# Kernel tuning notes

Hardware: AMD Instinct MI355X
Metric: run time of the kernel (lower is better)

## Reference

```python
import jax, jax.numpy as jnp
import numpy as np

NEG_SLOPE = 0.2
MASK_FILL = -1e9

N, F_IN, K, F_OUT = 4096, 512, 8, 128


def setup_inputs() -> dict:
    key = jax.random.key(0)
    k1, k2, k3, k4, k5 = jax.random.split(key, 5)
    x = jax.random.normal(k1, (N, F_IN), dtype=jnp.float32)
    mask = jax.random.randint(k2, (N, N), 0, 2).astype(jnp.bool_)
    # ensure no fully-masked row (self loops)
    mask = mask | jnp.eye(N, dtype=jnp.bool_)
    # xavier-ish scaled params
    W = jax.random.normal(k3, (K * F_OUT, F_IN), dtype=jnp.float32) * (2.0 / (F_IN + K * F_OUT)) ** 0.5
    b = jnp.zeros((K * F_OUT,), dtype=jnp.float32)
    a_left = jax.random.normal(k4, (K, F_OUT), dtype=jnp.float32) * (2.0 / (1 + F_OUT)) ** 0.5
    a_right = jax.random.normal(k5, (K, F_OUT), dtype=jnp.float32) * (2.0 / (1 + F_OUT)) ** 0.5
    return {"x": x, "mask": mask, "W": W, "b": b, "a_left": a_left, "a_right": a_right}


def reference(x, mask, W, b, a_left, a_right):
    # Linear projection: (N, K*F') -> (N, K, F')
    h = (x @ W.T + b).reshape(x.shape[0], K, F_OUT)
    # Additive attention logits: e[k,n,m] = leaky_relu(a_left.h_n + a_right.h_m)
    left = jnp.einsum('nkf,kf->kn', h, a_left)    # (K, N)
    right = jnp.einsum('mkf,kf->km', h, a_right)  # (K, N)
    e = jax.nn.leaky_relu(left[:, :, None] + right[:, None, :], NEG_SLOPE)  # (K,N,N)
    # Mask out non-neighbors, softmax over neighbor axis m
    e = jnp.where(mask[None, :, :], e, MASK_FILL)
    a = jax.nn.softmax(e, axis=-1)  # (K, N, N)
    # Weighted aggregation (eq. 4) + ELU
    h_prime = jax.nn.elu(jnp.einsum('knm,mkf->nkf', a, h))  # (N, K, F')
    # Concat heads (eq. 5): (N, K*F')
    return h_prime.reshape(h_prime.shape[0], -1)
```

## Files before the change

### kernel.cpp

```cpp
#include <hip/hip_runtime.h>
#include <hip/hip_bf16.h>

typedef unsigned short u16;
typedef __attribute__((ext_vector_type(8))) short short8;
typedef __attribute__((ext_vector_type(2))) float f32x2;
typedef __attribute__((ext_vector_type(4))) float f32x4;
typedef __attribute__((ext_vector_type(16))) float f32x16;

#define N_NODES 4096
#define FIN 512
#define KH 8
#define FO 128
#define DM 1024
#define LOG2E 1.44269504088896340736f

__device__ __forceinline__ void gload16(const u16* g, u16* l) {
    __builtin_amdgcn_global_load_lds(
        (const __attribute__((address_space(1))) unsigned int*)g,
        (__attribute__((address_space(3))) unsigned int*)l,
        16, 0, 0);
}

__device__ __forceinline__ unsigned pk_bf16(float lo, float hi) {
    unsigned r;
    asm("v_cvt_pk_bf16_f32 %0, %1, %2" : "=v"(r) : "v"(lo), "v"(hi));
    return r;
}

__device__ __forceinline__ float pkmul_max(f32x2 a, f32x2 b) {
    f32x2 r;
    asm("v_pk_mul_f32 %0, %1, %2" : "=v"(r) : "v"(a), "v"(b));
    return fmaxf(r.x, r.y);
}

__global__ __launch_bounds__(256) void split_bf16(const float* __restrict__ src,
                                                  u16* __restrict__ hi,
                                                  u16* __restrict__ lo,
                                                  int n4) {
    int idx = blockIdx.x * 256 + threadIdx.x;
    if (idx >= n4) return;
    float4 v = ((const float4*)src)[idx];
    unsigned h01 = pk_bf16(v.x, v.y);
    unsigned h23 = pk_bf16(v.z, v.w);
    float hx = __uint_as_float(h01 << 16);
    float hy = __uint_as_float(h01 & 0xffff0000u);
    float hz = __uint_as_float(h23 << 16);
    float hw = __uint_as_float(h23 & 0xffff0000u);
    unsigned l01 = pk_bf16(v.x - hx, v.y - hy);
    unsigned l23 = pk_bf16(v.z - hz, v.w - hw);
    uint2 hv; hv.x = h01; hv.y = h23;
    uint2 lv; lv.x = l01; lv.y = l23;
    ((uint2*)hi)[idx] = hv;
    ((uint2*)lo)[idx] = lv;
}

__global__ __launch_bounds__(512) void gemm_mfma(const u16* __restrict__ Xh,
                                                 const u16* __restrict__ Xl,
                                                 const u16* __restrict__ Wh,
                                                 const u16* __restrict__ Wl,
                                                 const float* __restrict__ bias,
                                                 const float* __restrict__ aL,
                                                 const float* __restrict__ aR,
                                                 float2* __restrict__ C2,
                                                 float2* __restrict__ D2,
                                                 u16* __restrict__ HbT) {
    const int khead = blockIdx.x;
    const int n0 = blockIdx.y * 128;
    const int tid = threadIdx.x;
    const int w = tid >> 6, lane = tid & 63;
    const int wr = w >> 1, wc = w & 1;
    const int c = lane & 31, half = lane >> 5;

    __shared__ u16 S[2][16384];

    const int sa = w >> 1;
    const int shv = w & 1;
    const int scl = lane & 3;
    const int ssw = ((lane >> 2) ^ (lane >> 4)) & 3;
    const int sgc = scl ^ ssw;
    const u16* gb; int growbase;
    if (sa == 0)      { gb = Xh; growbase = n0; }
    else if (sa == 1) { gb = Xl; growbase = n0; }
    else if (sa == 2) { gb = Wh; growbase = khead * 128; }
    else              { gb = Wl; growbase = khead * 128; }
    const u16* glb = gb + (size_t)(growbase + shv * 64 + (lane >> 2)) * FIN + sgc * 8;
    const int sldsoff = sa * 4096 + shv * 64 * 32;

    const int sw = ((c) ^ (c >> 2)) & 3;
    const int aoff = (wr * 32 + c) * 32;
    const int boff0 = 8192 + (wc * 64 + c) * 32;
    const int boff1 = 8192 + (wc * 64 + 32 + c) * 32;

    f32x16 acc0, acc1;
#pragma unroll
    for (int i = 0; i < 16; ++i) { acc0[i] = 0.f; acc1[i] = 0.f; }

#pragma unroll
    for (int i = 0; i < 4; ++i)
        gload16(glb + (size_t)i * 16 * FIN, &S[0][sldsoff + i * 512]);
    __syncthreads();

    int cur = 0;
    for (int kt = 0; kt < 16; ++kt) {
        if (kt < 15) {
            const u16* gsrc = glb + (kt + 1) * 32;
            u16* dst = &S[cur ^ 1][sldsoff];
#pragma unroll
            for (int i = 0; i < 4; ++i)
                gload16(gsrc + (size_t)i * 16 * FIN, dst + i * 512);
        }

        const u16* sp = S[cur];
        short8 ah[2], al8[2], bh[2][2], bl8[2][2];
#pragma unroll
        for (int ks = 0; ks < 2; ++ks) {
            int ch = ((ks * 2 + half) ^ sw) * 8;
            ah[ks]     = *(const short8*)&sp[aoff + ch];
            al8[ks]    = *(const short8*)&sp[4096 + aoff + ch];
            bh[0][ks]  = *(const short8*)&sp[boff0 + ch];
            bl8[0][ks] = *(const short8*)&sp[boff0 + 4096 + ch];
            bh[1][ks]  = *(const short8*)&sp[boff1 + ch];
            bl8[1][ks] = *(const short8*)&sp[boff1 + 4096 + ch];
        }
#pragma unroll
        for (int ks = 0; ks < 2; ++ks) {
            acc0 = __builtin_amdgcn_mfma_f32_32x32x16_bf16(ah[ks], bh[0][ks], acc0, 0, 0, 0);
            acc0 = __builtin_amdgcn_mfma_f32_32x32x16_bf16(ah[ks], bl8[0][ks], acc0, 0, 0, 0);
            acc0 = __builtin_amdgcn_mfma_f32_32x32x16_bf16(al8[ks], bh[0][ks], acc0, 0, 0, 0);
            acc1 = __builtin_amdgcn_mfma_f32_32x32x16_bf16(ah[ks], bh[1][ks], acc1, 0, 0, 0);
            acc1 = __builtin_amdgcn_mfma_f32_32x32x16_bf16(ah[ks], bl8[1][ks], acc1, 0, 0, 0);
            acc1 = __builtin_amdgcn_mfma_f32_32x32x16_bf16(al8[ks], bh[1][ks], acc1, 0, 0, 0);
        }
        __syncthreads();
        cur ^= 1;
    }

    const int fglob = khead * FO + wc * 64 + c;
    float b0 = bias[fglob], b1 = bias[fglob + 32];
#pragma unroll
    for (int r = 0; r < 16; ++r) { acc0[r] += b0; acc1[r] += b1; }

    float alv0 = aL[fglob], alv1 = aL[fglob + 32];
    float arv0 = aR[fglob], arv1 = aR[fglob + 32];
    float pl[16], pr[16];
#pragma unroll
    for (int r = 0; r < 16; ++r) {
        pl[r] = acc0[r] * alv0 + acc1[r] * alv1;
        pr[r] = acc0[r] * arv0 + acc1[r] * arv1;
    }
#pragma unroll
    for (int off = 1; off < 32; off <<= 1) {
#pragma unroll
        for (int r = 0; r < 16; ++r) {
            pl[r] += __shfl_xor(pl[r], off);
            pr[r] += __shfl_xor(pr[r], off);
        }
    }

    u16* T = &S[0][0];
    float* LRf = (float*)&S[0][0] + 9216;

    if (c == 0) {
#pragma unroll
        for (int r = 0; r < 16; ++r) {
            int node = wr * 32 + (r & 3) + 8 * (r >> 2) + 4 * half;
            LRf[(wc * 2 + 0) * 128 + node] = pl[r];
            LRf[(wc * 2 + 1) * 128 + node] = pr[r];
        }
    }

#pragma unroll
    for (int q = 0; q < 4; ++q) {
        int nb = wr * 32 + q * 8 + 4 * half;
        unsigned p00 = pk_bf16(acc0[q * 4 + 0], acc0[q * 4 + 1]);
        unsigned p01 = pk_bf16(acc0[q * 4 + 2], acc0[q * 4 + 3]);
        unsigned p10 = pk_bf16(acc1[q * 4 + 0], acc1[q * 4 + 1]);
        unsigned p11 = pk_bf16(acc1[q * 4 + 2], acc1[q * 4 + 3]);
        *(unsigned*)&T[(wc * 64 + c) * 136 + nb]      = p00;
        *(unsigned*)&T[(wc * 64 + c) * 136 + nb + 2]  = p01;
        *(unsigned*)&T[(wc * 64 + 32 + c) * 136 + nb]     = p10;
        *(unsigned*)&T[(wc * 64 + 32 + c) * 136 + nb + 2] = p11;
    }
    __syncthreads();

    if (wc == 0) {
        int node = wr * 32 + (lane & 31);
        if (lane < 32) {
            float L = (LRf[0 * 128 + node] + LRf[2 * 128 + node]) * LOG2E;
            float2 cv; cv.x = exp2f(L); cv.y = exp2f(0.2f * L);
            C2[(size_t)khead * N_NODES + n0 + node] = cv;
        } else {
            float R = (LRf[1 * 128 + node] + LRf[3 * 128 + node]) * LOG2E;
            float2 dv; dv.x = exp2f(R); dv.y = exp2f(0.2f * R);
            D2[(size_t)khead * N_NODES + n0 + node] = dv;
        }
    }

    {
        int f = tid >> 2, q = tid & 3;
        const uint4* src = (const uint4*)&T[f * 136 + q * 32];
        uint4* dst = (uint4*)(HbT + (size_t)(khead * FO + f) * N_NODES + n0 + q * 32);
#pragma unroll
        for (int u = 0; u < 4; ++u) dst[u] = src[u];
    }
}

__global__ __launch_bounds__(256) void pack_mask(const int* __restrict__ mask,
                                                 unsigned long long* __restrict__ mb) {
    int gid = blockIdx.x * 256 + threadIdx.x;
    int wid = gid >> 6, lane = gid & 63;
    int v = mask[(size_t)wid * 64 + lane];
    unsigned long long bits = __ballot(v != 0);
    if (lane == 0) mb[wid] = bits;
}

__global__ __launch_bounds__(512) void gat_attn(const u16* __restrict__ HbT,
                                                const float2* __restrict__ C2,
                                                const float2* __restrict__ D2,
                                                const unsigned long long* __restrict__ mb,
                                                float* __restrict__ out) {
    const int k = blockIdx.y;
    const int n0 = blockIdx.x * 64;
    const int tid = threadIdx.x;
    const int w = tid >> 6, lane = tid & 63;
    const int g = w >> 2, wg = w & 3;
    const int fr = lane & 15, kg = lane >> 4;

    __shared__ u16 Ht[2][2][128 * 64];

    const int n_a = n0 + wg * 16 + fr;
    const float2 ccf = C2[(size_t)k * N_NODES + n_a];
    f32x2 cc; cc.x = ccf.x; cc.y = ccf.y;
    const unsigned long long* mrow = mb + (size_t)n_a * 64 + g * 32;

    f32x4 acc[9];
#pragma unroll
    for (int c = 0; c < 9; ++c) acc[c] = 0.f;

    const short o1 = (fr == 0) ? (short)0x3F80 : (short)0;
    const short8 ones = {o1, o1, o1, o1, o1, o1, o1, o1};

    const int fsub = lane >> 3;
    const int seg = ((lane & 7) ^ fsub) * 8;
    const u16* gstage = HbT + (size_t)(k * FO + wg * 32 + fsub) * N_NODES + g * 2048 + seg;
    u16* lb0 = &Ht[g][0][wg * 2048];
    u16* lb1 = &Ht[g][1][wg * 2048];

    const int frx = fr & 7;
    const int off0 = fr * 64 + (kg ^ frx) * 8;
    const int off1 = fr * 64 + ((kg + 4) ^ frx) * 8;

    const float2* D2k = D2 + (size_t)k * N_NODES + g * 2048 + kg * 8;

#pragma unroll
    for (int j = 0; j < 4; ++j)
        gload16(gstage + (size_t)j * 8 * N_NODES, lb0 + j * 512);
    __syncthreads();

    int cur = 0;
    for (int mt = 0; mt < 32; ++mt) {
        const int m0 = mt * 64;

        union { float4 f4[4]; f32x2 f2[8]; } Da, Db;
        {
            const float4* dva = (const float4*)(D2k + m0);
            const float4* dvb = (const float4*)(D2k + m0 + 32);
#pragma unroll
            for (int i = 0; i < 4; ++i) { Da.f4[i] = dva[i]; Db.f4[i] = dvb[i]; }
        }
        unsigned long long bits = mrow[mt];
        __builtin_amdgcn_sched_barrier(0);

        if (mt < 31) {
            u16* nb = cur ? lb0 : lb1;
            const u16* gs = gstage + m0 + 64;
#pragma unroll
            for (int j = 0; j < 4; ++j)
                gload16(gs + (size_t)j * 8 * N_NODES, nb + j * 512);
        }
        __builtin_amdgcn_sched_barrier(0);

        unsigned m32a = (unsigned)(bits >> (kg * 8));
        unsigned m32b = (unsigned)(bits >> (kg * 8 + 32));
        float p0[8], p1[8];
#pragma unroll
        for (int v = 0; v < 8; ++v) {
            float pa = pkmul_max(cc, Da.f2[v]);
            unsigned sa2 = (unsigned)(((int)(m32a << (31 - v))) >> 31);
            p0[v] = __uint_as_float(__float_as_uint(pa) & sa2);
            float pb = pkmul_max(cc, Db.f2[v]);
            unsigned sb2 = (unsigned)(((int)(m32b << (31 - v))) >> 31);
            p1[v] = __uint_as_float(__float_as_uint(pb) & sb2);
        }
        union { unsigned u[4]; short8 s; } ua, ub;
#pragma unroll
        for (int vp = 0; vp < 4; ++vp) {
            ua.u[vp] = pk_bf16(p0[2 * vp], p0[2 * vp + 1]);
            ub.u[vp] = pk_bf16(p1[2 * vp], p1[2 * vp + 1]);
        }
        short8 a0 = ua.s, a1 = ub.s;

        const u16* hb = &Ht[g][cur][0];
#pragma unroll
        for (int c = 0; c < 8; ++c) {
            short8 b0 = *(const short8*)(hb + c * 1024 + off0);
            short8 b1 = *(const short8*)(hb + c * 1024 + off1);
            acc[c] = __builtin_amdgcn_mfma_f32_16x16x32_bf16(a0, b0, acc[c], 0, 0, 0);
            acc[c] = __builtin_amdgcn_mfma_f32_16x16x32_bf16(a1, b1, acc[c], 0, 0, 0);
        }
        acc[8] = __builtin_amdgcn_mfma_f32_16x16x32_bf16(a0, ones, acc[8], 0, 0, 0);
        acc[8] = __builtin_amdgcn_mfma_f32_16x16x32_bf16(a1, ones, acc[8], 0, 0, 0);

        __syncthreads();
        cur ^= 1;
    }

    float* cmb = (float*)&Ht[0][0][0];
    if (g == 1) {
        float* base = cmb + wg * (36 * 64);
#pragma unroll
        for (int c = 0; c < 9; ++c)
#pragma unroll
            for (int j = 0; j < 4; ++j) base[(c * 4 + j) * 64 + lane] = acc[c][j];
    }
    __syncthreads();
    if (g == 0) {
        const float* base = cmb + wg * (36 * 64);
#pragma unroll
        for (int c = 0; c < 9; ++c)
#pragma unroll
            for (int j = 0; j < 4; ++j) acc[c][j] += base[(c * 4 + j) * 64 + lane];

#pragma unroll
        for (int j = 0; j < 4; ++j) {
            float S = __shfl(acc[8][j], (lane & 48));
            float inv = 1.0f / S;
            int n_out = n0 + wg * 16 + kg * 4 + j;
            float* orow = out + (size_t)n_out * DM + k * FO + fr;
#pragma unroll
            for (int c = 0; c < 8; ++c) {
                float v = acc[c][j] * inv;
                float e = v > 0.f ? v : (__expf(v) - 1.0f);
                orow[c * 16] = e;
            }
        }
    }
}

extern "C" void kernel_launch(void* const* d_in, const int* in_sizes, int n_in,
                              void* d_out, int out_size, void* d_ws, size_t ws_size,
                              hipStream_t stream) {
    const float* x = (const float*)d_in[0];
    const int* mask = (const int*)d_in[1];
    const float* W = (const float*)d_in[2];
    const float* bias = (const float*)d_in[3];
    const float* aL = (const float*)d_in[4];
    const float* aR = (const float*)d_in[5];
    float* out = (float*)d_out;

    char* ws = (char*)d_ws;
    u16* Xh = (u16*)ws;   ws += (size_t)N_NODES * FIN * 2;
    u16* Xl = (u16*)ws;   ws += (size_t)N_NODES * FIN * 2;
    u16* Wh = (u16*)ws;   ws += (size_t)DM * FIN * 2;
    u16* Wl = (u16*)ws;   ws += (size_t)DM * FIN * 2;
    u16* HbT = (u16*)ws;  ws += (size_t)KH * FO * N_NODES * 2;
    float2* C2 = (float2*)ws;  ws += (size_t)KH * N_NODES * 8;
    float2* D2 = (float2*)ws;  ws += (size_t)KH * N_NODES * 8;
    unsigned long long* mb = (unsigned long long*)ws;

    split_bf16<<<dim3(2048), dim3(256), 0, stream>>>(x, Xh, Xl, N_NODES * FIN / 4);
    split_bf16<<<dim3(512), dim3(256), 0, stream>>>(W, Wh, Wl, DM * FIN / 4);
    gemm_mfma<<<dim3(8, 32), dim3(512), 0, stream>>>(Xh, Xl, Wh, Wl, bias, aL, aR,
                                                     C2, D2, HbT);
    pack_mask<<<dim3(65536), dim3(256), 0, stream>>>(mask, mb);
    gat_attn<<<dim3(64, 8), dim3(512), 0, stream>>>(HbT, C2, D2, mb, out);
}
```

Baseline: 133.0 us.

## Deepen attention pipeline with prefetched bf16 D factors and reordered block mapping

The attention kernel now stores the right-side exponential factors as packed bf16 instead of float2, which halves their load traffic. It prefetches those factors and the mask bits one tile ahead in registers, and issues the LDS staging loads two tiles ahead with explicit vmcnt waits and split barriers. The block index is remapped so all eight heads of a node tile are adjacent, which should improve L2 reuse of the mask, and a minimum-occupancy launch bound is added. The cost is lower precision on the D factors, more register pressure, and fragile hand-coded waitcnt counts.

```diff
diff --git a/kernel.cpp b/kernel.cpp
--- a/kernel.cpp
+++ b/kernel.cpp
@@ -62,7 +62,7 @@
                                                  const float* __restrict__ aL,
                                                  const float* __restrict__ aR,
                                                  float2* __restrict__ C2,
-                                                 float2* __restrict__ D2,
+                                                 unsigned* __restrict__ D2b,
                                                  u16* __restrict__ HbT) {
     const int khead = blockIdx.x;
     const int n0 = blockIdx.y * 128;
@@ -191,8 +191,7 @@
             C2[(size_t)khead * N_NODES + n0 + node] = cv;
         } else {
             float R = (LRf[1 * 128 + node] + LRf[3 * 128 + node]) * LOG2E;
-            float2 dv; dv.x = exp2f(R); dv.y = exp2f(0.2f * R);
-            D2[(size_t)khead * N_NODES + n0 + node] = dv;
+            D2b[(size_t)khead * N_NODES + n0 + node] = pk_bf16(exp2f(R), exp2f(0.2f * R));
         }
     }
 
@@ -214,13 +213,44 @@
     if (lane == 0) mb[wid] = bits;
 }
 
-__global__ __launch_bounds__(512) void gat_attn(const u16* __restrict__ HbT,
-                                                const float2* __restrict__ C2,
-                                                const float2* __restrict__ D2,
-                                                const unsigned long long* __restrict__ mb,
-                                                float* __restrict__ out) {
-    const int k = blockIdx.y;
-    const int n0 = blockIdx.x * 64;
+__device__ __forceinline__ void pgen(f32x2 cc, uint4 a0v, uint4 a1v, uint4 b0v, uint4 b1v,
+                                     unsigned long long bits, int kg,
+                                     short8& A0, short8& A1) {
+    unsigned m32a = (unsigned)(bits >> (kg * 8));
+    unsigned m32b = (unsigned)(bits >> (kg * 8 + 32));
+    unsigned dua[8] = {a0v.x, a0v.y, a0v.z, a0v.w, a1v.x, a1v.y, a1v.z, a1v.w};
+    unsigned dub[8] = {b0v.x, b0v.y, b0v.z, b0v.w, b1v.x, b1v.y, b1v.z, b1v.w};
+    float p0[8], p1[8];
+#pragma unroll
+    for (int v = 0; v < 8; ++v) {
+        f32x2 dva; dva.x = __uint_as_float(dua[v] << 16);
+        dva.y = __uint_as_float(dua[v] & 0xffff0000u);
+        float pa = pkmul_max(cc, dva);
+        unsigned sa2 = (unsigned)(((int)(m32a << (31 - v))) >> 31);
+        p0[v] = __uint_as_float(__float_as_uint(pa) & sa2);
+        f32x2 dvb; dvb.x = __uint_as_float(dub[v] << 16);
+        dvb.y = __uint_as_float(dub[v] & 0xffff0000u);
+        float pb = pkmul_max(cc, dvb);
+        unsigned sb2 = (unsigned)(((int)(m32b << (31 - v))) >> 31);
+        p1[v] = __uint_as_float(__float_as_uint(pb) & sb2);
+    }
+    union { unsigned u[4]; short8 s; } ua, ub;
+#pragma unroll
+    for (int vp = 0; vp < 4; ++vp) {
+        ua.u[vp] = pk_bf16(p0[2 * vp], p0[2 * vp + 1]);
+        ub.u[vp] = pk_bf16(p1[2 * vp], p1[2 * vp + 1]);
+    }
+    A0 = ua.s; A1 = ub.s;
+}
+
+__global__ __launch_bounds__(512, 4) void gat_attn(const u16* __restrict__ HbT,
+                                                   const float2* __restrict__ C2,
+                                                   const unsigned* __restrict__ D2b,
+                                                   const unsigned long long* __restrict__ mb,
+                                                   float* __restrict__ out) {
+    const int blk = blockIdx.x;
+    const int k = blk & 7;
+    const int n0 = (blk >> 3) * 64;
     const int tid = threadIdx.x;
     const int w = tid >> 6, lane = tid & 63;
     const int g = w >> 2, wg = w & 3;
@@ -250,70 +280,69 @@
     const int off0 = fr * 64 + (kg ^ frx) * 8;
     const int off1 = fr * 64 + ((kg + 4) ^ frx) * 8;
 
-    const float2* D2k = D2 + (size_t)k * N_NODES + g * 2048 + kg * 8;
-
+    const unsigned* D2k = D2b + (size_t)k * N_NODES + g * 2048 + kg * 8;
+
+    uint4 dA0, dA1, dB0, dB1, eA0, eA1, eB0, eB1;
+    unsigned long long bc, bn;
+    dA0 = *(const uint4*)(D2k);      dA1 = *(const uint4*)(D2k + 4);
+    dB0 = *(const uint4*)(D2k + 32); dB1 = *(const uint4*)(D2k + 36);
+    bc = mrow[0];
+    __builtin_amdgcn_sched_barrier(0);
 #pragma unroll
     for (int j = 0; j < 4; ++j)
         gload16(gstage + (size_t)j * 8 * N_NODES, lb0 + j * 512);
+    __builtin_amdgcn_sched_barrier(0);
+#pragma unroll
+    for (int j = 0; j < 4; ++j)
+        gload16(gstage + 64 + (size_t)j * 8 * N_NODES, lb1 + j * 512);
+    __builtin_amdgcn_sched_barrier(0);
+    asm volatile("s_waitcnt vmcnt(4)" ::: "memory");
+    __builtin_amdgcn_sched_barrier(0);
+    __builtin_amdgcn_s_barrier();
+    __builtin_amdgcn_sched_barrier(0);
+
+#define ATTN_STEP(BUF, MT, DA0,DA1,DB0,DB1,BITS, NA0,NA1,NB0,NB1,NBITS)  do {          \
+    short8 a0, a1;                                                                      \
+    pgen(cc, DA0, DA1, DB0, DB1, BITS, kg, a0, a1);                                     \
+    __builtin_amdgcn_sched_barrier(0);                                                  \
+    { const unsigned* dnp = D2k + ((((MT) + 1) & 31) << 6);                             \
+      NA0 = *(const uint4*)(dnp);      NA1 = *(const uint4*)(dnp + 4);                  \
+      NB0 = *(const uint4*)(dnp + 32); NB1 = *(const uint4*)(dnp + 36);                 \
+      NBITS = mrow[((MT) + 1) & 31]; }                                                  \
+    __builtin_amdgcn_sched_barrier(0);                                                  \
+    { const u16* hb = &Ht[g][BUF][0];                                                   \
+      _Pragma("unroll")                                                                 \
+      for (int c = 0; c < 8; ++c) {                                                     \
+          short8 b0 = *(const short8*)(hb + c * 1024 + off0);                           \
+          short8 b1 = *(const short8*)(hb + c * 1024 + off1);                           \
+          acc[c] = __builtin_amdgcn_mfma_f32_16x16x32_bf16(a0, b0, acc[c], 0, 0, 0);    \
+          acc[c] = __builtin_amdgcn_mfma_f32_16x16x32_bf16(a1, b1, acc[c], 0, 0, 0);    \
+      }                                                                                 \
+      acc[8] = __builtin_amdgcn_mfma_f32_16x16x32_bf16(a0, ones, acc[8], 0, 0, 0);      \
+      acc[8] = __builtin_amdgcn_mfma_f32_16x16x32_bf16(a1, ones, acc[8], 0, 0, 0); }    \
+    asm volatile("s_waitcnt lgkmcnt(0)" ::: "memory");                                  \
+    __builtin_amdgcn_sched_barrier(0);                                                  \
+    __builtin_amdgcn_s_barrier();                                                       \
+    __builtin_amdgcn_sched_barrier(0);                                                  \
+    { const u16* gs = gstage + ((((MT) + 2) & 31) << 6);                                \
+      u16* lbs = (BUF) ? lb1 : lb0;                                                     \
+      _Pragma("unroll")                                                                 \
+      for (int j = 0; j < 4; ++j)                                                       \
+          gload16(gs + (size_t)j * 8 * N_NODES, lbs + j * 512); }                       \
+    __builtin_amdgcn_sched_barrier(0);                                                  \
+    asm volatile("s_waitcnt vmcnt(9)" ::: "memory");                                    \
+    __builtin_amdgcn_sched_barrier(0);                                                  \
+    __builtin_amdgcn_s_barrier();                                                       \
+    __builtin_amdgcn_sched_barrier(0);                                                  \
+} while (0)
+
+    for (int mt = 0; mt < 32; mt += 2) {
+        ATTN_STEP(0, mt,     dA0, dA1, dB0, dB1, bc,  eA0, eA1, eB0, eB1, bn);
+        ATTN_STEP(1, mt + 1, eA0, eA1, eB0, eB1, bn,  dA0, dA1, dB0, dB1, bc);
+    }
+#undef ATTN_STEP
+
     __syncthreads();
-
-    int cur = 0;
-    for (int mt = 0; mt < 32; ++mt) {
-        const int m0 = mt * 64;
-
-        union { float4 f4[4]; f32x2 f2[8]; } Da, Db;
-        {
-            const float4* dva = (const float4*)(D2k + m0);
-            const float4* dvb = (const float4*)(D2k + m0 + 32);
-#pragma unroll
-            for (int i = 0; i < 4; ++i) { Da.f4[i] = dva[i]; Db.f4[i] = dvb[i]; }
-        }
-        unsigned long long bits = mrow[mt];
-        __builtin_amdgcn_sched_barrier(0);
-
-        if (mt < 31) {
-            u16* nb = cur ? lb0 : lb1;
-            const u16* gs = gstage + m0 + 64;
-#pragma unroll
-            for (int j = 0; j < 4; ++j)
-                gload16(gs + (size_t)j * 8 * N_NODES, nb + j * 512);
-        }
-        __builtin_amdgcn_sched_barrier(0);
-
-        unsigned m32a = (unsigned)(bits >> (kg * 8));
-        unsigned m32b = (unsigned)(bits >> (kg * 8 + 32));
-        float p0[8], p1[8];
-#pragma unroll
-        for (int v = 0; v < 8; ++v) {
-            float pa = pkmul_max(cc, Da.f2[v]);
-            unsigned sa2 = (unsigned)(((int)(m32a << (31 - v))) >> 31);
-            p0[v] = __uint_as_float(__float_as_uint(pa) & sa2);
-            float pb = pkmul_max(cc, Db.f2[v]);
-            unsigned sb2 = (unsigned)(((int)(m32b << (31 - v))) >> 31);
-            p1[v] = __uint_as_float(__float_as_uint(pb) & sb2);
-        }
-        union { unsigned u[4]; short8 s; } ua, ub;
-#pragma unroll
-        for (int vp = 0; vp < 4; ++vp) {
-            ua.u[vp] = pk_bf16(p0[2 * vp], p0[2 * vp + 1]);
-            ub.u[vp] = pk_bf16(p1[2 * vp], p1[2 * vp + 1]);
-        }
-        short8 a0 = ua.s, a1 = ub.s;
-
-        const u16* hb = &Ht[g][cur][0];
-#pragma unroll
-        for (int c = 0; c < 8; ++c) {
-            short8 b0 = *(const short8*)(hb + c * 1024 + off0);
-            short8 b1 = *(const short8*)(hb + c * 1024 + off1);
-            acc[c] = __builtin_amdgcn_mfma_f32_16x16x32_bf16(a0, b0, acc[c], 0, 0, 0);
-            acc[c] = __builtin_amdgcn_mfma_f32_16x16x32_bf16(a1, b1, acc[c], 0, 0, 0);
-        }
-        acc[8] = __builtin_amdgcn_mfma_f32_16x16x32_bf16(a0, ones, acc[8], 0, 0, 0);
-        acc[8] = __builtin_amdgcn_mfma_f32_16x16x32_bf16(a1, ones, acc[8], 0, 0, 0);
-
-        __syncthreads();
-        cur ^= 1;
-    }
 
     float* cmb = (float*)&Ht[0][0][0];
     if (g == 1) {
@@ -365,13 +394,13 @@
     u16* Wl = (u16*)ws;   ws += (size_t)DM * FIN * 2;
     u16* HbT = (u16*)ws;  ws += (size_t)KH * FO * N_NODES * 2;
     float2* C2 = (float2*)ws;  ws += (size_t)KH * N_NODES * 8;
-    float2* D2 = (float2*)ws;  ws += (size_t)KH * N_NODES * 8;
+    unsigned* D2b = (unsigned*)ws; ws += (size_t)KH * N_NODES * 4;
     unsigned long long* mb = (unsigned long long*)ws;
 
     split_bf16<<<dim3(2048), dim3(256), 0, stream>>>(x, Xh, Xl, N_NODES * FIN / 4);
     split_bf16<<<dim3(512), dim3(256), 0, stream>>>(W, Wh, Wl, DM * FIN / 4);
     gemm_mfma<<<dim3(8, 32), dim3(512), 0, stream>>>(Xh, Xl, Wh, Wl, bias, aL, aR,
-                                                     C2, D2, HbT);
+                                                     C2, D2b, HbT);
     pack_mask<<<dim3(65536), dim3(256), 0, stream>>>(mask, mb);
-    gat_attn<<<dim3(64, 8), dim3(512), 0, stream>>>(HbT, C2, D2, mb, out);
-}
+    gat_attn<<<dim3(512), dim3(512), 0, stream>>>(HbT, C2, D2b, mb, out);
+}
```

Result: no change. 131.7 us (-0.9%).

## Restructure GAT attention kernel: 4-way neighbor split, shared B tiles, scalar row sums

Applied to the files above, without the earlier changes.

Reworks gat_attn so the 8 waves form 4 neighbor-range groups × 2 node-halves. Each wave computes two 16-row node subtiles that share each LDS B fragment, so one LDS read feeds two MFMAs. The softmax denominator is now accumulated as scalar sums instead of an extra 'ones' MFMA. The grid becomes 1D with heads interleaved and launch_bounds requests 4 waves/SIMD occupancy. The cost is a 3-round cross-group LDS reduction at the end and a redundant wrap-around prefetch on the last iteration.

```diff
diff --git a/kernel.cpp b/kernel.cpp
--- a/kernel.cpp
+++ b/kernel.cpp
@@ -191,8 +191,8 @@
             C2[(size_t)khead * N_NODES + n0 + node] = cv;
         } else {
             float R = (LRf[1 * 128 + node] + LRf[3 * 128 + node]) * LOG2E;
-            float2 dv; dv.x = exp2f(R); dv.y = exp2f(0.2f * R);
-            D2[(size_t)khead * N_NODES + n0 + node] = dv;
+            float2 dvv; dvv.x = exp2f(R); dvv.y = exp2f(0.2f * R);
+            D2[(size_t)khead * N_NODES + n0 + node] = dvv;
         }
     }
 
@@ -214,83 +214,79 @@
     if (lane == 0) mb[wid] = bits;
 }
 
-__global__ __launch_bounds__(512) void gat_attn(const u16* __restrict__ HbT,
-                                                const float2* __restrict__ C2,
-                                                const float2* __restrict__ D2,
-                                                const unsigned long long* __restrict__ mb,
-                                                float* __restrict__ out) {
-    const int k = blockIdx.y;
-    const int n0 = blockIdx.x * 64;
+__global__ __launch_bounds__(512, 4) void gat_attn(const u16* __restrict__ HbT,
+                                                   const float2* __restrict__ C2,
+                                                   const float2* __restrict__ D2,
+                                                   const unsigned* __restrict__ M32,
+                                                   float* __restrict__ out) {
+    const int blk = blockIdx.x;
+    const int k = blk & 7;
+    const int n0 = (blk >> 3) * 64;
     const int tid = threadIdx.x;
     const int w = tid >> 6, lane = tid & 63;
-    const int g = w >> 2, wg = w & 3;
+    const int ns = w & 1, g = w >> 1;
     const int fr = lane & 15, kg = lane >> 4;
 
-    __shared__ u16 Ht[2][2][128 * 64];
-
-    const int n_a = n0 + wg * 16 + fr;
-    const float2 ccf = C2[(size_t)k * N_NODES + n_a];
-    f32x2 cc; cc.x = ccf.x; cc.y = ccf.y;
-    const unsigned long long* mrow = mb + (size_t)n_a * 64 + g * 32;
-
-    f32x4 acc[9];
-#pragma unroll
-    for (int c = 0; c < 9; ++c) acc[c] = 0.f;
-
-    const short o1 = (fr == 0) ? (short)0x3F80 : (short)0;
-    const short8 ones = {o1, o1, o1, o1, o1, o1, o1, o1};
-
-    const int fsub = lane >> 3;
-    const int seg = ((lane & 7) ^ fsub) * 8;
-    const u16* gstage = HbT + (size_t)(k * FO + wg * 32 + fsub) * N_NODES + g * 2048 + seg;
-    u16* lb0 = &Ht[g][0][wg * 2048];
-    u16* lb1 = &Ht[g][1][wg * 2048];
-
-    const int frx = fr & 7;
-    const int off0 = fr * 64 + (kg ^ frx) * 8;
-    const int off1 = fr * 64 + ((kg + 4) ^ frx) * 8;
-
-    const float2* D2k = D2 + (size_t)k * N_NODES + g * 2048 + kg * 8;
+    __shared__ u16 Ht[4][2][4096];
+
+    const int na0 = n0 + ns * 32 + fr;
+    const int na1 = na0 + 16;
+    float2 c0f = C2[(size_t)k * N_NODES + na0];
+    float2 c1f = C2[(size_t)k * N_NODES + na1];
+    f32x2 cc0; cc0.x = c0f.x; cc0.y = c0f.y;
+    f32x2 cc1; cc1.x = c1f.x; cc1.y = c1f.y;
+    const unsigned* mrow0 = M32 + (size_t)na0 * 128 + g * 32;
+    const unsigned* mrow1 = M32 + (size_t)na1 * 128 + g * 32;
+
+    f32x4 acc[2][8];
+#pragma unroll
+    for (int s = 0; s < 2; ++s)
+#pragma unroll
+        for (int c = 0; c < 8; ++c) acc[s][c] = 0.f;
+    float S0 = 0.f, S1 = 0.f;
+
+    const int srow = lane >> 2;
+    const int gch = (lane & 3) ^ ((lane >> 3) & 3);
+    const u16* gsb = HbT + (size_t)(k * FO + ns * 64 + srow) * N_NODES + g * 1024 + gch * 8;
+    u16* ldsw = &Ht[g][0][ns * 2048];
+
+    const int offb = fr * 32 + ((kg ^ ((fr >> 1) & 3)) << 3);
+    const float2* Dk = D2 + (size_t)k * N_NODES + g * 1024 + kg * 8;
 
 #pragma unroll
     for (int j = 0; j < 4; ++j)
-        gload16(gstage + (size_t)j * 8 * N_NODES, lb0 + j * 512);
-    __syncthreads();
-
-    int cur = 0;
+        gload16(gsb + (size_t)j * 16 * N_NODES, ldsw + j * 512);
+    asm volatile("s_waitcnt vmcnt(0)" ::: "memory");
+    __builtin_amdgcn_s_barrier();
+
     for (int mt = 0; mt < 32; ++mt) {
-        const int m0 = mt * 64;
-
-        union { float4 f4[4]; f32x2 f2[8]; } Da, Db;
+        const int cur = mt & 1;
+        const float4* dp = (const float4*)(Dk + mt * 32);
+        float4 dq0 = dp[0], dq1 = dp[1], dq2 = dp[2], dq3 = dp[3];
+        unsigned mw0 = mrow0[mt], mw1 = mrow1[mt];
         {
-            const float4* dva = (const float4*)(D2k + m0);
-            const float4* dvb = (const float4*)(D2k + m0 + 32);
-#pragma unroll
-            for (int i = 0; i < 4; ++i) { Da.f4[i] = dva[i]; Db.f4[i] = dvb[i]; }
-        }
-        unsigned long long bits = mrow[mt];
+            const u16* gs = gsb + (((mt + 1) & 31) << 5);
+            u16* ld = ldsw + ((cur ^ 1) << 12);
+#pragma unroll
+            for (int j = 0; j < 4; ++j)
+                gload16(gs + (size_t)j * 16 * N_NODES, ld + j * 512);
+        }
         __builtin_amdgcn_sched_barrier(0);
 
-        if (mt < 31) {
-            u16* nb = cur ? lb0 : lb1;
-            const u16* gs = gstage + m0 + 64;
-#pragma unroll
-            for (int j = 0; j < 4; ++j)
-                gload16(gs + (size_t)j * 8 * N_NODES, nb + j * 512);
-        }
-        __builtin_amdgcn_sched_barrier(0);
-
-        unsigned m32a = (unsigned)(bits >> (kg * 8));
-        unsigned m32b = (unsigned)(bits >> (kg * 8 + 32));
+        float dv[16] = {dq0.x, dq0.y, dq0.z, dq0.w, dq1.x, dq1.y, dq1.z, dq1.w,
+                        dq2.x, dq2.y, dq2.z, dq2.w, dq3.x, dq3.y, dq3.z, dq3.w};
+        unsigned mq0 = mw0 >> (kg * 8);
+        unsigned mq1 = mw1 >> (kg * 8);
         float p0[8], p1[8];
 #pragma unroll
         for (int v = 0; v < 8; ++v) {
-            float pa = pkmul_max(cc, Da.f2[v]);
-            unsigned sa2 = (unsigned)(((int)(m32a << (31 - v))) >> 31);
-            p0[v] = __uint_as_float(__float_as_uint(pa) & sa2);
-            float pb = pkmul_max(cc, Db.f2[v]);
-            unsigned sb2 = (unsigned)(((int)(m32b << (31 - v))) >> 31);
-            p1[v] = __uint_as_float(__float_as_uint(pb) & sb2);
+            f32x2 dd; dd.x = dv[2 * v]; dd.y = dv[2 * v + 1];
+            float pa = pkmul_max(cc0, dd);
+            float pb = pkmul_max(cc1, dd);
+            unsigned s0 = (unsigned)(((int)(mq0 << (31 - v))) >> 31);
+            unsigned s1 = (unsigned)(((int)(mq1 << (31 - v))) >> 31);
+            p0[v] = __uint_as_float(__float_as_uint(pa) & s0);
+            p1[v] = __uint_as_float(__float_as_uint(pb) & s1);
         }
         union { unsigned u[4]; short8 s; } ua, ub;
 #pragma unroll
@@ -299,49 +295,69 @@
             ub.u[vp] = pk_bf16(p1[2 * vp], p1[2 * vp + 1]);
         }
         short8 a0 = ua.s, a1 = ub.s;
+#pragma unroll
+        for (int v = 0; v < 8; ++v) { S0 += p0[v]; S1 += p1[v]; }
 
         const u16* hb = &Ht[g][cur][0];
 #pragma unroll
         for (int c = 0; c < 8; ++c) {
-            short8 b0 = *(const short8*)(hb + c * 1024 + off0);
-            short8 b1 = *(const short8*)(hb + c * 1024 + off1);
-            acc[c] = __builtin_amdgcn_mfma_f32_16x16x32_bf16(a0, b0, acc[c], 0, 0, 0);
-            acc[c] = __builtin_amdgcn_mfma_f32_16x16x32_bf16(a1, b1, acc[c], 0, 0, 0);
-        }
-        acc[8] = __builtin_amdgcn_mfma_f32_16x16x32_bf16(a0, ones, acc[8], 0, 0, 0);
-        acc[8] = __builtin_amdgcn_mfma_f32_16x16x32_bf16(a1, ones, acc[8], 0, 0, 0);
-
+            short8 b = *(const short8*)(hb + c * 512 + offb);
+            acc[0][c] = __builtin_amdgcn_mfma_f32_16x16x32_bf16(a0, b, acc[0][c], 0, 0, 0);
+            acc[1][c] = __builtin_amdgcn_mfma_f32_16x16x32_bf16(a1, b, acc[1][c], 0, 0, 0);
+        }
+        asm volatile("s_waitcnt lgkmcnt(0)" ::: "memory");
+        asm volatile("s_waitcnt vmcnt(0)" ::: "memory");
+        __builtin_amdgcn_s_barrier();
+    }
+
+    __syncthreads();
+
+    float* fb = (float*)&Ht[0][0][0];
+    const int cbase = ns * (66 * 64) + lane;
+    for (int src = 1; src < 4; ++src) {
+        if (g == src) {
+#pragma unroll
+            for (int s = 0; s < 2; ++s)
+#pragma unroll
+                for (int c = 0; c < 8; ++c)
+#pragma unroll
+                    for (int j = 0; j < 4; ++j)
+                        fb[cbase + (((s * 8 + c) * 4 + j) << 6)] = acc[s][c][j];
+            fb[cbase + (64 << 6)] = S0;
+            fb[cbase + (65 << 6)] = S1;
+        }
         __syncthreads();
-        cur ^= 1;
-    }
-
-    float* cmb = (float*)&Ht[0][0][0];
-    if (g == 1) {
-        float* base = cmb + wg * (36 * 64);
-#pragma unroll
-        for (int c = 0; c < 9; ++c)
-#pragma unroll
-            for (int j = 0; j < 4; ++j) base[(c * 4 + j) * 64 + lane] = acc[c][j];
-    }
-    __syncthreads();
+        if (g == 0) {
+#pragma unroll
+            for (int s = 0; s < 2; ++s)
+#pragma unroll
+                for (int c = 0; c < 8; ++c)
+#pragma unroll
+                    for (int j = 0; j < 4; ++j)
+                        acc[s][c][j] += fb[cbase + (((s * 8 + c) * 4 + j) << 6)];
+            S0 += fb[cbase + (64 << 6)];
+            S1 += fb[cbase + (65 << 6)];
+        }
+        __syncthreads();
+    }
+
     if (g == 0) {
-        const float* base = cmb + wg * (36 * 64);
-#pragma unroll
-        for (int c = 0; c < 9; ++c)
-#pragma unroll
-            for (int j = 0; j < 4; ++j) acc[c][j] += base[(c * 4 + j) * 64 + lane];
-
-#pragma unroll
-        for (int j = 0; j < 4; ++j) {
-            float S = __shfl(acc[8][j], (lane & 48));
-            float inv = 1.0f / S;
-            int n_out = n0 + wg * 16 + kg * 4 + j;
-            float* orow = out + (size_t)n_out * DM + k * FO + fr;
-#pragma unroll
-            for (int c = 0; c < 8; ++c) {
-                float v = acc[c][j] * inv;
-                float e = v > 0.f ? v : (__expf(v) - 1.0f);
-                orow[c * 16] = e;
+        S0 += __shfl_xor(S0, 16); S0 += __shfl_xor(S0, 32);
+        S1 += __shfl_xor(S1, 16); S1 += __shfl_xor(S1, 32);
+#pragma unroll
+        for (int s = 0; s < 2; ++s) {
+#pragma unroll
+            for (int j = 0; j < 4; ++j) {
+                float Srow = __shfl(s == 0 ? S0 : S1, kg * 4 + j);
+                float inv = 1.0f / Srow;
+                int n_out = n0 + ns * 32 + s * 16 + kg * 4 + j;
+                float* orow = out + (size_t)n_out * DM + k * FO + fr;
+#pragma unroll
+                for (int c = 0; c < 8; ++c) {
+                    float vv = acc[s][c][j] * inv;
+                    float e = vv > 0.f ? vv : (__expf(vv) - 1.0f);
+                    orow[c * 16] = e;
+                }
             }
         }
     }
@@ -373,5 +389,5 @@
     gemm_mfma<<<dim3(8, 32), dim3(512), 0, stream>>>(Xh, Xl, Wh, Wl, bias, aL, aR,
                                                      C2, D2, HbT);
     pack_mask<<<dim3(65536), dim3(256), 0, stream>>>(mask, mb);
-    gat_attn<<<dim3(64, 8), dim3(512), 0, stream>>>(HbT, C2, D2, mb, out);
-}
+    gat_attn<<<dim3(512), dim3(512), 0, stream>>>(HbT, C2, D2, (const unsigned*)mb, out);
+}
```

After: 139.5 us. +5.0%, slower.
